# Kernel tuning notes

Measured on AMD Instinct MI355X. Metric: run time of the kernel, lower is better.

## Reference

```python
import jax, jax.numpy as jnp
import numpy as np

B, N, K, H = 4, 2048, 30, 128
NODE_IN, EDGE_IN, FF = 21, 16, 4 * H


def _normalize(t, axis=-1):
    d = t / jnp.linalg.norm(t, axis=axis, keepdims=True)
    return jnp.where(jnp.isnan(d), 0.0, d)


def gather_nodes(nodes, idx):
    # nodes: [B,N,C], idx: [B,N,K] -> [B,N,K,C]
    b, n, k = idx.shape
    flat = idx.reshape(b, n * k)
    out = jnp.take_along_axis(nodes, flat[:, :, None], axis=1)
    return out.reshape(b, n, k, nodes.shape[-1])


def cal_dihedral(Xf, eps=1e-7):
    dX = Xf[:, 1:, :] - Xf[:, :-1, :]
    U = _normalize(dX)
    u0, u1, u2 = U[:, :-2], U[:, 1:-1], U[:, 2:]
    n0 = _normalize(jnp.cross(u0, u1))
    n1 = _normalize(jnp.cross(u1, u2))
    cosD = jnp.clip((n0 * n1).sum(-1), -1 + eps, 1 - eps)
    v = _normalize(jnp.cross(n0, n1))
    return jnp.sign((-v * u1).sum(-1)) * jnp.arccos(cosD)


def dihedrals(X, eps=1e-7):
    b, n = X.shape[0], X.shape[1]
    Xf = X[:, :, :3, :].reshape(b, 3 * n, 3)
    D = cal_dihedral(Xf)
    D = jnp.pad(D, ((0, 0), (1, 2))).reshape(b, n, 3)
    dihed = jnp.concatenate([jnp.cos(D), jnp.sin(D)], -1)
    dX = Xf[:, 1:] - Xf[:, :-1]
    U = _normalize(dX)
    cosA = jnp.clip((U[:, :-2] * U[:, 1:-1]).sum(-1), -1 + eps, 1 - eps)
    A = jnp.pad(jnp.arccos(cosA), ((0, 0), (1, 2))).reshape(b, n, 3)
    ang = jnp.concatenate([jnp.cos(A), jnp.sin(A)], -1)
    return jnp.concatenate([dihed, ang], -1)  # [B,N,12]


def quaternions(R):
    diag = jnp.diagonal(R, axis1=-2, axis2=-1)
    Rxx, Ryy, Rzz = diag[..., 0], diag[..., 1], diag[..., 2]
    mags = 0.5 * jnp.sqrt(jnp.abs(1 + jnp.stack([Rxx - Ryy - Rzz, -Rxx + Ryy - Rzz, -Rxx - Ryy + Rzz], -1)))
    signs = jnp.sign(jnp.stack([R[..., 2, 1] - R[..., 1, 2], R[..., 0, 2] - R[..., 2, 0], R[..., 1, 0] - R[..., 0, 1]], -1))
    xyz = signs * mags
    w = jnp.sqrt(jax.nn.relu(1 + diag.sum(-1, keepdims=True))) / 2.0
    return _normalize(jnp.concatenate([xyz, w], -1))


def orientations(X, E_idx):
    V = X  # [B,N,4,3]
    b, n = X.shape[0], X.shape[1]
    k = E_idx.shape[2]
    Xf = X[:, :, :3, :].reshape(b, 3 * n, 3)
    dX = Xf[:, 1:] - Xf[:, :-1]
    U = _normalize(dX)
    u0, u1 = U[:, :-2], U[:, 1:-1]
    n0 = _normalize(jnp.cross(u0, u1))[:, ::3]
    b1 = _normalize(u0 - u1)[:, ::3]
    Xa = Xf[:, ::3]  # [B,N,3]
    Q = jnp.stack([b1, n0, jnp.cross(b1, n0)], 2)  # [B,N-1,3,3]
    Q = Q.reshape(b, Q.shape[1], 9)
    Q = jnp.pad(Q, ((0, 0), (0, 1), (0, 0)))  # [B,N,9]
    Qn = gather_nodes(Q, E_idx).reshape(b, n, k, 3, 3)
    Xn = gather_nodes(V[:, :, 1, :], E_idx)
    Nn = gather_nodes(V[:, :, 0, :], E_idx)
    Cn = gather_nodes(V[:, :, 2, :], E_idx)
    On = gather_nodes(V[:, :, 3, :], E_idx)
    Q3 = Q.reshape(b, n, 3, 3)
    dXn = jnp.stack([Xn, Nn, Cn, On], 3) - Xa[:, :, None, None, :]  # [B,N,K,4,3]
    dU = jnp.einsum('bnij,bnkaj->bnkai', Q3, dXn)
    E_direct = _normalize(dU).reshape(b, n, k, 12)
    R = jnp.einsum('bnji,bnkjl->bnkil', Q3, Qn)  # Q^T @ Q_neighbors
    q = quaternions(R)  # [B,N,K,4]
    dX_inner = V[:, :, jnp.array([0, 2, 3]), :] - Xa[:, :, None, :]
    dU_inner = _normalize(jnp.einsum('bnij,bnaj->bnai', Q3, dX_inner))
    V_direct = dU_inner.reshape(b, n, 9)
    return V_direct, E_direct, q


def layernorm(x, g, bta, eps=1e-5):
    m = x.mean(-1, keepdims=True)
    v = ((x - m) ** 2).mean(-1, keepdims=True)
    return (x - m) / jnp.sqrt(v + eps) * g + bta


def gelu(x):
    return jax.nn.gelu(x, approximate=False)


def forward(X, E_idx, Wv_w, Wv_b, We_w, We_b, W1_w, W1_b, W2_w, W2_b, W3_w, W3_b,
            Wi_w, Wi_b, Wo_w, Wo_b, ln1_g, ln1_b, ln2_g, ln2_b):
    k = E_idx.shape[2]
    Dfeat = dihedrals(X)                     # [B,N,12]
    Vd, Ed, q = orientations(X, E_idx)       # [B,N,9],[B,N,K,12],[B,N,K,4]
    hV = jnp.concatenate([Dfeat, Vd], -1) @ Wv_w + Wv_b     # [B,N,H]
    hE = jnp.concatenate([Ed, q], -1) @ We_w + We_b         # [B,N,K,H]
    hV_nbr = gather_nodes(hV, E_idx)                        # [B,N,K,H]
    hV_exp = jnp.broadcast_to(hV[:, :, None, :], hV_nbr.shape)
    hEV = jnp.concatenate([hV_exp, hE, hV_nbr], -1)         # [B,N,K,3H]
    msg = gelu(hEV @ W1_w + W1_b)
    msg = gelu(msg @ W2_w + W2_b)
    msg = msg @ W3_w + W3_b
    dh = msg.sum(-2) / k
    hV = layernorm(hV + dh, ln1_g, ln1_b)
    ff = gelu(hV @ Wi_w + Wi_b) @ Wo_w + Wo_b
    hV = layernorm(hV + ff, ln2_g, ln2_b)
    return hV


def _lin(key, fan_in, fan_out):
    s = 1.0 / np.sqrt(fan_in)
    kw, kb = jax.random.split(key)
    return (jax.random.uniform(kw, (fan_in, fan_out), minval=-s, maxval=s),
            jax.random.uniform(kb, (fan_out,), minval=-s, maxval=s))


def setup_inputs() -> dict:
    key = jax.random.key(0)
    ks = jax.random.split(key, 10)
    X = jax.random.normal(ks[0], (B, N, 4, 3), dtype=jnp.float32) * 3.0
    E_idx = jax.random.randint(ks[1], (B, N, K), 0, N)
    Wv_w, Wv_b = _lin(ks[2], NODE_IN, H)
    We_w, We_b = _lin(ks[3], EDGE_IN, H)
    W1_w, W1_b = _lin(ks[4], 3 * H, H)
    W2_w, W2_b = _lin(ks[5], H, H)
    W3_w, W3_b = _lin(ks[6], H, H)
    Wi_w, Wi_b = _lin(ks[7], H, FF)
    Wo_w, Wo_b = _lin(ks[8], FF, H)
    return {
        'X': X, 'E_idx': E_idx,
        'Wv_w': Wv_w, 'Wv_b': Wv_b, 'We_w': We_w, 'We_b': We_b,
        'W1_w': W1_w, 'W1_b': W1_b, 'W2_w': W2_w, 'W2_b': W2_b,
        'W3_w': W3_w, 'W3_b': W3_b, 'Wi_w': Wi_w, 'Wi_b': Wi_b,
        'Wo_w': Wo_w, 'Wo_b': Wo_b,
        'ln1_g': jnp.ones((H,), jnp.float32), 'ln1_b': jnp.zeros((H,), jnp.float32),
        'ln2_g': jnp.ones((H,), jnp.float32), 'ln2_b': jnp.zeros((H,), jnp.float32),
    }


def reference(X, E_idx, Wv_w, Wv_b, We_w, We_b, W1_w, W1_b, W2_w, W2_b, W3_w, W3_b,
              Wi_w, Wi_b, Wo_w, Wo_b, ln1_g, ln1_b, ln2_g, ln2_b):
    return forward(X, E_idx, Wv_w, Wv_b, We_w, We_b, W1_w, W1_b, W2_w, W2_b,
                   W3_w, W3_b, Wi_w, Wi_b, Wo_w, Wo_b, ln1_g, ln1_b, ln2_g, ln2_b)
```

## Files before the change

### kernel.cpp

```cpp
#include <hip/hip_runtime.h>
#include <math.h>

#define BB 4
#define NN 2048
#define KNB 30
#define HH 128
#define FFD 512

typedef __attribute__((ext_vector_type(4))) float  f32x4;
typedef __attribute__((ext_vector_type(8))) short  s16x8;
typedef __attribute__((ext_vector_type(4))) short  s16x4;

struct F3 { float x,y,z; };
__device__ __forceinline__ F3 f3(float a,float b,float c){ F3 r; r.x=a; r.y=b; r.z=c; return r; }
__device__ __forceinline__ F3 sub3(F3 a, F3 b){ return f3(a.x-b.x, a.y-b.y, a.z-b.z); }
__device__ __forceinline__ float dot3(F3 a, F3 b){ return a.x*b.x + a.y*b.y + a.z*b.z; }
__device__ __forceinline__ F3 cross3(F3 a, F3 b){
  return f3(a.y*b.z-a.z*b.y, a.z*b.x-a.x*b.z, a.x*b.y-a.y*b.x);
}
__device__ __forceinline__ F3 nrm3(F3 a){
  float n2 = dot3(a,a);
  if (n2 <= 0.f) return f3(0.f,0.f,0.f);
  float inv = 1.0f/sqrtf(n2);
  return f3(a.x*inv, a.y*inv, a.z*inv);
}
__device__ __forceinline__ float sgnf(float x){ return (x>0.f)?1.f:((x<0.f)?-1.f:0.f); }
__device__ __forceinline__ float clip1(float x){
  const float e = 1e-7f;
  return fminf(fmaxf(x, -1.f+e), 1.f-e);
}
__device__ __forceinline__ float fgelu(float x){
  float x2 = x*x;
  float t = __builtin_fmaf(-0.1029641763f, x2, -2.302344055f);
  float d = 1.f + __builtin_amdgcn_exp2f(t*x);
  return x * __builtin_amdgcn_rcpf(d);
}
__device__ __forceinline__ short f2bf(float x){
  union { float f; unsigned u; } v; v.f = x;
  unsigned r = v.u + 0x7fffu + ((v.u >> 16) & 1u);
  return (short)(r >> 16);
}

__global__ void k_init(const float* __restrict__ X, float* __restrict__ Qws,
                       float* __restrict__ featws,
                       const float* __restrict__ We, const float* __restrict__ Web,
                       const float* __restrict__ W1, const float* __restrict__ W2,
                       const float* __restrict__ Wi, const float* __restrict__ Wo,
                       short* __restrict__ wfoldT, float* __restrict__ bfold,
                       short* __restrict__ w2t, short* __restrict__ w1aT,
                       short* __restrict__ w1cT, short* __restrict__ wiT,
                       short* __restrict__ woT){
  if (blockIdx.x < 32){
    int t = blockIdx.x*256 + threadIdx.x;
    int b = t / NN, n = t % NN;
    const float* Xb = X + (size_t)b*NN*12;
    #define LD3(r,a) f3(Xb[((r)*4+(a))*3+0], Xb[((r)*4+(a))*3+1], Xb[((r)*4+(a))*3+2])
    F3 x0=LD3(n,0), x1=LD3(n,1), x2=LD3(n,2), x3=LD3(n,3);
    F3 U[5];
    U[1]=nrm3(sub3(x1,x0));
    U[2]=nrm3(sub3(x2,x1));
    if (n>0){ F3 p = LD3(n-1,2); U[0]=nrm3(sub3(x0,p)); } else U[0]=f3(0.f,0.f,0.f);
    if (n<NN-1){ F3 y0=LD3(n+1,0), y1=LD3(n+1,1); U[3]=nrm3(sub3(y0,x2)); U[4]=nrm3(sub3(y1,y0)); }
    else { U[3]=f3(0.f,0.f,0.f); U[4]=f3(0.f,0.f,0.f); }

    float feat[21];
    #pragma unroll
    for (int tt=0; tt<3; tt++){
      bool valid = (n>0 || tt>0) && (n<NN-1 || tt==0);
      if (valid){
        F3 a=U[tt], bv=U[tt+1], c=U[tt+2];
        F3 n0=nrm3(cross3(a,bv)), n1=nrm3(cross3(bv,c));
        float cd = clip1(dot3(n0,n1));
        F3 v = nrm3(cross3(n0,n1));
        float s = sgnf(-dot3(v,bv));
        feat[tt]   = (s==0.f) ? 1.f : cd;
        feat[3+tt] = s*sqrtf(fmaxf(1.f-cd*cd, 0.f));
        float ca = clip1(dot3(a,bv));
        feat[6+tt] = ca;
        feat[9+tt] = sqrtf(fmaxf(1.f-ca*ca, 0.f));
      } else {
        feat[tt]=1.f; feat[3+tt]=0.f; feat[6+tt]=1.f; feat[9+tt]=0.f;
      }
    }
    float Q[9];
    if (n<NN-1){
      F3 b1=nrm3(sub3(U[1],U[2]));
      F3 n0=nrm3(cross3(U[1],U[2]));
      F3 r2=cross3(b1,n0);
      Q[0]=b1.x;Q[1]=b1.y;Q[2]=b1.z;Q[3]=n0.x;Q[4]=n0.y;Q[5]=n0.z;Q[6]=r2.x;Q[7]=r2.y;Q[8]=r2.z;
    } else {
      #pragma unroll
      for (int i=0;i<9;i++) Q[i]=0.f;
    }
    float* qp = Qws + (size_t)t*9;
    #pragma unroll
    for (int i=0;i<9;i++) qp[i]=Q[i];

    feat[12]=0.f; feat[13]=0.f; feat[14]=0.f;
    F3 d1=sub3(x2,x0), d2=sub3(x3,x0);
    F3 r1 = nrm3(f3(Q[0]*d1.x+Q[1]*d1.y+Q[2]*d1.z,
                    Q[3]*d1.x+Q[4]*d1.y+Q[5]*d1.z,
                    Q[6]*d1.x+Q[7]*d1.y+Q[8]*d1.z));
    F3 r2v= nrm3(f3(Q[0]*d2.x+Q[1]*d2.y+Q[2]*d2.z,
                    Q[3]*d2.x+Q[4]*d2.y+Q[5]*d2.z,
                    Q[6]*d2.x+Q[7]*d2.y+Q[8]*d2.z));
    feat[15]=r1.x; feat[16]=r1.y; feat[17]=r1.z;
    feat[18]=r2v.x; feat[19]=r2v.y; feat[20]=r2v.z;
    float* fp = featws + (size_t)t*21;
    #pragma unroll
    for (int i=0;i<21;i++) fp[i]=feat[i];
    #undef LD3
    return;
  }
  int t = (blockIdx.x-32)*256 + threadIdx.x;
  if (t < 2048){
    int c = t >> 4, j = t & 15;
    float a = 0.f;
    for (int k=0;k<HH;k++) a += We[j*HH+k]*W1[(HH+k)*HH + c];
    wfoldT[t] = f2bf(a);
  } else if (t < 2176){
    int c = t - 2048;
    float a = 0.f;
    for (int k=0;k<HH;k++) a += Web[k]*W1[(HH+k)*HH + c];
    bfold[c] = a;
  } else if (t < 18560){
    int i = t - 2176;  int n = i >> 7, k = i & 127;
    w2t[n*HH + k] = f2bf(W2[k*HH + n]);
  } else if (t < 34944){
    int i = t - 18560; int n = i >> 7, k = i & 127;
    w1aT[n*HH + k] = f2bf(W1[k*HH + n]);
  } else if (t < 51328){
    int i = t - 34944; int n = i >> 7, k = i & 127;
    w1cT[n*HH + k] = f2bf(W1[(256+k)*HH + n]);
  } else if (t < 116864){
    int i = t - 51328; int n = i >> 7, k = i & 127;
    wiT[n*HH + k] = f2bf(Wi[k*FFD + n]);
  } else if (t < 182400){
    int i = t - 116864; int k = i >> 7, n = i & 127;
    woT[n*FFD + k] = f2bf(Wo[k*HH + n]);
  }
}

#define PNB 32
__global__ void k_pre(const float* __restrict__ featws, const float* __restrict__ Wv,
                      const float* __restrict__ Wvb, const short* __restrict__ w1aT,
                      const short* __restrict__ w1cT, const float* __restrict__ W1b,
                      const float* __restrict__ bfold, float* __restrict__ hVws,
                      float* __restrict__ Sws, float* __restrict__ Gws){
  __shared__ __align__(16) short hvL[PNB][136];
  int tid = threadIdx.x;
  int base = blockIdx.x*PNB;
  {
    int c = tid & 127, half = tid >> 7;
    float wv[21];
    #pragma unroll
    for (int j=0;j<21;j++) wv[j] = Wv[j*HH + c];
    float wb = Wvb[c];
    #pragma unroll 2
    for (int it=0; it<16; ++it){
      int g = it*2 + half;
      const float* f = featws + (size_t)(base+g)*21;
      float a = wb;
      #pragma unroll
      for (int j=0;j<21;j++) a += f[j]*wv[j];
      hVws[(size_t)(base+g)*HH + c] = a;
      hvL[g][c] = f2bf(a);
    }
  }
  __syncthreads();
  {
    int l = tid & 63, w = tid >> 6;
    int lr = l & 15, lg = l >> 4;
    int m = w & 1;
    int nbase = (w >> 1)*4;
    s16x8 afr[4];
    #pragma unroll
    for (int ks=0; ks<4; ks++)
      afr[ks] = *reinterpret_cast<const s16x8*>(&hvL[m*16 + lr][ks*32 + lg*8]);
    f32x4 Cs[4], Cg[4];
    #pragma unroll
    for (int q=0;q<4;q++){ Cs[q]=(f32x4){0,0,0,0}; Cg[q]=(f32x4){0,0,0,0}; }
    #pragma unroll
    for (int q=0;q<4;q++){
      int ncol = (nbase+q)*16 + lr;
      #pragma unroll
      for (int ks=0; ks<4; ks++){
        s16x8 ba = *reinterpret_cast<const s16x8*>(&w1aT[ncol*HH + ks*32 + lg*8]);
        s16x8 bc = *reinterpret_cast<const s16x8*>(&w1cT[ncol*HH + ks*32 + lg*8]);
        Cs[q] = __builtin_amdgcn_mfma_f32_16x16x32_bf16(afr[ks], ba, Cs[q], 0,0,0);
        Cg[q] = __builtin_amdgcn_mfma_f32_16x16x32_bf16(afr[ks], bc, Cg[q], 0,0,0);
      }
    }
    #pragma unroll
    for (int q=0;q<4;q++){
      int ncol = (nbase+q)*16 + lr;
      float bc = W1b[ncol] + bfold[ncol];
      #pragma unroll
      for (int i=0;i<4;i++){
        int row = m*16 + lg*4 + i;
        size_t o = (size_t)(base+row)*HH + ncol;
        Sws[o] = Cs[q][i] + bc;
        Gws[o] = Cg[q][i];
      }
    }
  }
}

#define NPB 4
#define A2STR 136
#define EFSTR 20
__launch_bounds__(256, 4)
__global__ void k_msg(const float* __restrict__ X, const int* __restrict__ Eidx,
                      const float* __restrict__ Qws, const float* __restrict__ Sws,
                      const float* __restrict__ Gws, const float* __restrict__ hVws,
                      const short* __restrict__ wfoldT, const short* __restrict__ w2t,
                      const float* __restrict__ W2b, const float* __restrict__ W3,
                      const float* __restrict__ W3b, float* __restrict__ xpre){
  __shared__ __align__(16) short efL[128*EFSTR];
  __shared__ int idxL[128];
  __shared__ __align__(16) short A2s[128*A2STR];
  float* csL = (float*)efL;

  const int tid = threadIdx.x;
  const int gbase = blockIdx.x*NPB;
  const int b = gbase >> 11;
  const int bofs = b*NN;

  if (tid < NPB*KNB){
    int nn = tid / KNB;
    int kk = tid - nn*KNB;
    int gnode = gbase + nn;
    int n = gnode - bofs;
    int j = Eidx[(size_t)gnode*KNB + kk];
    int r = nn*32 + kk;
    idxL[r] = j;
    const float* Qs = Qws + (size_t)gnode*9;
    float q[9];
    #pragma unroll
    for (int i=0;i<9;i++) q[i]=Qs[i];
    const float* Xb = X + (size_t)b*NN*12;
    F3 Xa = f3(Xb[n*12+0], Xb[n*12+1], Xb[n*12+2]);
    const float* Xn = Xb + (size_t)j*12;
    F3 A[4];
    A[0] = f3(Xn[3],  Xn[4],  Xn[5]);
    A[1] = f3(Xn[0],  Xn[1],  Xn[2]);
    A[2] = f3(Xn[6],  Xn[7],  Xn[8]);
    A[3] = f3(Xn[9],  Xn[10], Xn[11]);
    #pragma unroll
    for (int a=0;a<4;a++){
      F3 d = sub3(A[a], Xa);
      F3 w = f3(q[0]*d.x+q[1]*d.y+q[2]*d.z,
                q[3]*d.x+q[4]*d.y+q[5]*d.z,
                q[6]*d.x+q[7]*d.y+q[8]*d.z);
      F3 wn = nrm3(w);
      efL[r*EFSTR + a*3 + 0] = f2bf(wn.x);
      efL[r*EFSTR + a*3 + 1] = f2bf(wn.y);
      efL[r*EFSTR + a*3 + 2] = f2bf(wn.z);
    }
    const float* Qn = Qws + (size_t)(bofs + j)*9;
    float p[9];
    #pragma unroll
    for (int i=0;i<9;i++) p[i]=Qn[i];
    float R00=q[0]*p[0]+q[3]*p[3]+q[6]*p[6];
    float R01=q[0]*p[1]+q[3]*p[4]+q[6]*p[7];
    float R02=q[0]*p[2]+q[3]*p[5]+q[6]*p[8];
    float R10=q[1]*p[0]+q[4]*p[3]+q[7]*p[6];
    float R11=q[1]*p[1]+q[4]*p[4]+q[7]*p[7];
    float R12=q[1]*p[2]+q[4]*p[5]+q[7]*p[8];
    float R20=q[2]*p[0]+q[5]*p[3]+q[8]*p[6];
    float R21=q[2]*p[1]+q[5]*p[4]+q[8]*p[7];
    float R22=q[2]*p[2]+q[5]*p[5]+q[8]*p[8];
    float mx = 0.5f*sqrtf(fabsf(1.f+R00-R11-R22));
    float my = 0.5f*sqrtf(fabsf(1.f-R00+R11-R22));
    float mz = 0.5f*sqrtf(fabsf(1.f-R00-R11+R22));
    float qx = sgnf(R21-R12)*mx;
    float qy = sgnf(R02-R20)*my;
    float qz = sgnf(R10-R01)*mz;
    float qw = 0.5f*sqrtf(fmaxf(1.f+R00+R11+R22, 0.f));
    float n2 = qx*qx+qy*qy+qz*qz+qw*qw;
    float inv = (n2>0.f) ? 1.f/sqrtf(n2) : 0.f;
    efL[r*EFSTR+12]=f2bf(qx*inv); efL[r*EFSTR+13]=f2bf(qy*inv);
    efL[r*EFSTR+14]=f2bf(qz*inv); efL[r*EFSTR+15]=f2bf(qw*inv);
  } else if (tid < 128){
    int e = tid - 120;
    int nn = e >> 1, slot = 30 + (e & 1);
    int r = nn*32 + slot;
    idxL[r] = 0;
    #pragma unroll
    for (int j2=0;j2<16;j2++) efL[r*EFSTR + j2] = 0;
  }
  __syncthreads();

  const int w  = tid >> 6;
  const int l  = tid & 63;
  const int lr = l & 15;
  const int lg = l >> 4;

  {
    s16x8 wf[8];
    #pragma unroll
    for (int ct=0; ct<8; ct++){
      if (lg < 2)
        wf[ct] = *reinterpret_cast<const s16x8*>(&wfoldT[(ct*16+lr)*16 + lg*8]);
      else
        wf[ct] = (s16x8){0,0,0,0,0,0,0,0};
    }
    s16x8 ef[2];
    #pragma unroll
    for (int rt=0; rt<2; rt++){
      if (lg < 2){
        const short* p = &efL[(w*32 + rt*16 + lr)*EFSTR + lg*8];
        s16x4 lo = *reinterpret_cast<const s16x4*>(p);
        s16x4 hi = *reinterpret_cast<const s16x4*>(p+4);
        s16x8 v;
        #pragma unroll
        for (int j2=0;j2<4;j2++){ v[j2]=lo[j2]; v[4+j2]=hi[j2]; }
        ef[rt] = v;
      } else {
        ef[rt] = (s16x8){0,0,0,0,0,0,0,0};
      }
    }
    const int e0 = w*32 + lr;
    const int e1 = e0 + 16;
    const bool ok1 = (lr < KNB - 16);
    const float* g0 = Gws + (size_t)(bofs + idxL[e0])*HH;
    const float* g1 = Gws + (size_t)(bofs + idxL[e1])*HH;
    const float* Srow = Sws + (size_t)(gbase+w)*HH;
    #pragma unroll
    for (int ct=0; ct<8; ct++){
      const int cbase = ct*16 + lg*4;
      f32x4 S4 = *reinterpret_cast<const f32x4*>(Srow + cbase);
      f32x4 G0 = *reinterpret_cast<const f32x4*>(g0 + cbase);
      f32x4 G1 = *reinterpret_cast<const f32x4*>(g1 + cbase);
      f32x4 C0 = __builtin_amdgcn_mfma_f32_16x16x32_bf16(wf[ct], ef[0], (f32x4){0,0,0,0}, 0,0,0);
      f32x4 C1 = __builtin_amdgcn_mfma_f32_16x16x32_bf16(wf[ct], ef[1], (f32x4){0,0,0,0}, 0,0,0);
      s16x4 o0, o1;
      #pragma unroll
      for (int i=0;i<4;i++){
        o0[i] = f2bf(fgelu(C0[i] + S4[i] + G0[i]));
        float v1 = fgelu(C1[i] + S4[i] + G1[i]);
        o1[i] = ok1 ? f2bf(v1) : (short)0;
      }
      *reinterpret_cast<s16x4*>(&A2s[e0*A2STR + cbase]) = o0;
      *reinterpret_cast<s16x4*>(&A2s[e1*A2STR + cbase]) = o1;
    }
  }
  __syncthreads();

  {
    f32x4 Cacc[2][8];
    #pragma unroll
    for (int mt=0; mt<2; mt++)
      #pragma unroll
      for (int nt=0; nt<8; nt++)
        Cacc[mt][nt] = (f32x4){0.f,0.f,0.f,0.f};
    #pragma unroll
    for (int ks=0; ks<4; ks++){
      const int koff = ks*32 + lg*8;
      s16x8 a0 = *reinterpret_cast<const s16x8*>(&A2s[(w*32      + lr)*A2STR + koff]);
      s16x8 a1 = *reinterpret_cast<const s16x8*>(&A2s[(w*32 + 16 + lr)*A2STR + koff]);
      #pragma unroll
      for (int nt=0; nt<8; nt++){
        s16x8 bv = *reinterpret_cast<const s16x8*>(&w2t[(lr + nt*16)*HH + koff]);
        Cacc[0][nt] = __builtin_amdgcn_mfma_f32_16x16x32_bf16(a0, bv, Cacc[0][nt], 0,0,0);
        Cacc[1][nt] = __builtin_amdgcn_mfma_f32_16x16x32_bf16(a1, bv, Cacc[1][nt], 0,0,0);
      }
    }
    #pragma unroll
    for (int nt=0; nt<8; nt++){
      float b2v = W2b[lr + nt*16];
      float part = 0.f;
      #pragma unroll
      for (int mt=0; mt<2; mt++){
        #pragma unroll
        for (int i=0; i<4; i++){
          int row32 = mt*16 + lg*4 + i;
          float v = fgelu(Cacc[mt][nt][i] + b2v);
          if (row32 < KNB) part += v;
        }
      }
      part += __shfl_xor(part, 16, 64);
      part += __shfl_xor(part, 32, 64);
      if (l < 16) csL[w*HH + nt*16 + lr] = part;
    }
  }
  __syncthreads();

  {
    const int h = tid & 127;
    const int half = tid >> 7;
    #pragma unroll
    for (int q2=0; q2<2; q2++){
      int nn = half*2 + q2;
      const float* cs = csL + nn*HH;
      float acc = 0.f;
      for (int j=0;j<HH;j+=4){
        acc += cs[j]  *W3[(j  )*HH+h] + cs[j+1]*W3[(j+1)*HH+h]
             + cs[j+2]*W3[(j+2)*HH+h] + cs[j+3]*W3[(j+3)*HH+h];
      }
      size_t o = (size_t)(gbase + nn)*HH + h;
      xpre[o] = hVws[o] + acc*(1.f/30.f) + W3b[h];
    }
  }
}

#define FNB 16
__global__ void k_ffn(const float* __restrict__ xpre, const short* __restrict__ wiT,
                      const short* __restrict__ woT, const float* __restrict__ Wib,
                      const float* __restrict__ Wob, const float* __restrict__ l1g,
                      const float* __restrict__ l1b, const float* __restrict__ l2g,
                      const float* __restrict__ l2b, float* __restrict__ out){
  __shared__ __align__(16) short hv1[FNB][136];
  __shared__ __align__(16) float yL[FNB][HH];
  __shared__ __align__(16) short ffh[FNB][520];
  __shared__ float partS[FNB][4], partQ[FNB][4];
  const int tid = threadIdx.x;
  const int l = tid & 63, w = tid >> 6;
  const int base = blockIdx.x*FNB;

  #pragma unroll
  for (int ri=0; ri<4; ri++){
    int r = w*4 + ri;
    const float* xp = xpre + (size_t)(base+r)*HH;
    float x0 = xp[l], x1 = xp[l+64];
    float s = x0 + x1;
    #pragma unroll
    for (int o=32;o>0;o>>=1) s += __shfl_xor(s, o, 64);
    float mean = s*(1.f/HH);
    float d0 = x0-mean, d1 = x1-mean;
    float q = d0*d0 + d1*d1;
    #pragma unroll
    for (int o=32;o>0;o>>=1) q += __shfl_xor(q, o, 64);
    float inv = 1.f/sqrtf(q*(1.f/HH) + 1e-5f);
    float y0 = d0*inv*l1g[l]    + l1b[l];
    float y1 = d1*inv*l1g[l+64] + l1b[l+64];
    yL[r][l] = y0; yL[r][l+64] = y1;
    hv1[r][l] = f2bf(y0); hv1[r][l+64] = f2bf(y1);
  }
  __syncthreads();

  const int lr = l & 15, lg = l >> 4;
  {
    s16x8 afr[4];
    #pragma unroll
    for (int ks=0; ks<4; ks++)
      afr[ks] = *reinterpret_cast<const s16x8*>(&hv1[lr][ks*32 + lg*8]);
    #pragma unroll
    for (int q=0; q<8; q++){
      int ncol = (w*8+q)*16 + lr;
      f32x4 C = (f32x4){0,0,0,0};
      #pragma unroll
      for (int ks=0; ks<4; ks++){
        s16x8 bv = *reinterpret_cast<const s16x8*>(&wiT[ncol*HH + ks*32 + lg*8]);
        C = __builtin_amdgcn_mfma_f32_16x16x32_bf16(afr[ks], bv, C, 0,0,0);
      }
      float bi = Wib[ncol];
      #pragma unroll
      for (int i=0;i<4;i++){
        int row = lg*4 + i;
        ffh[row][ncol] = f2bf(fgelu(C[i] + bi));
      }
    }
  }
  __syncthreads();

  f32x4 C2[2];
  C2[0]=(f32x4){0,0,0,0}; C2[1]=(f32x4){0,0,0,0};
  for (int ks=0; ks<16; ++ks){
    s16x8 a = *reinterpret_cast<const s16x8*>(&ffh[lr][ks*32 + lg*8]);
    #pragma unroll
    for (int t2=0; t2<2; t2++){
      int ncol = (2*w+t2)*16 + lr;
      s16x8 bv = *reinterpret_cast<const s16x8*>(&woT[ncol*FFD + ks*32 + lg*8]);
      C2[t2] = __builtin_amdgcn_mfma_f32_16x16x32_bf16(a, bv, C2[t2], 0,0,0);
    }
  }
  float vv[2][4];
  float ps[4] = {0,0,0,0}, pq[4] = {0,0,0,0};
  #pragma unroll
  for (int t2=0; t2<2; t2++){
    int col = (2*w+t2)*16 + lr;
    float bo = Wob[col];
    #pragma unroll
    for (int i=0;i<4;i++){
      int row = lg*4 + i;
      float v = yL[row][col] + C2[t2][i] + bo;
      vv[t2][i] = v;
      ps[i] += v; pq[i] += v*v;
    }
  }
  #pragma unroll
  for (int i=0;i<4;i++){
    #pragma unroll
    for (int o=1;o<16;o<<=1){
      ps[i] += __shfl_xor(ps[i], o, 64);
      pq[i] += __shfl_xor(pq[i], o, 64);
    }
    if (lr == 0){ partS[lg*4+i][w] = ps[i]; partQ[lg*4+i][w] = pq[i]; }
  }
  __syncthreads();
  float mean[4], inv[4];
  #pragma unroll
  for (int i=0;i<4;i++){
    int row = lg*4 + i;
    float S = partS[row][0]+partS[row][1]+partS[row][2]+partS[row][3];
    float Q = partQ[row][0]+partQ[row][1]+partQ[row][2]+partQ[row][3];
    float m = S*(1.f/HH);
    float var = Q*(1.f/HH) - m*m;
    mean[i] = m;
    inv[i] = 1.f/sqrtf(var + 1e-5f);
  }
  #pragma unroll
  for (int t2=0; t2<2; t2++){
    int col = (2*w+t2)*16 + lr;
    float g2 = l2g[col], b2 = l2b[col];
    #pragma unroll
    for (int i=0;i<4;i++){
      int row = lg*4 + i;
      out[(size_t)(base+row)*HH + col] = (vv[t2][i]-mean[i])*inv[i]*g2 + b2;
    }
  }
}

extern "C" void kernel_launch(void* const* d_in, const int* in_sizes, int n_in,
                              void* d_out, int out_size, void* d_ws, size_t ws_size,
                              hipStream_t stream) {
  (void)in_sizes; (void)n_in; (void)out_size; (void)ws_size;
  const float* X   = (const float*)d_in[0];
  const int*   Ei  = (const int*)  d_in[1];
  const float* Wv  = (const float*)d_in[2];
  const float* Wvb = (const float*)d_in[3];
  const float* We  = (const float*)d_in[4];
  const float* Web = (const float*)d_in[5];
  const float* W1  = (const float*)d_in[6];
  const float* W1b = (const float*)d_in[7];
  const float* W2  = (const float*)d_in[8];
  const float* W2b = (const float*)d_in[9];
  const float* W3  = (const float*)d_in[10];
  const float* W3b = (const float*)d_in[11];
  const float* Wi  = (const float*)d_in[12];
  const float* Wib = (const float*)d_in[13];
  const float* Wo  = (const float*)d_in[14];
  const float* Wob = (const float*)d_in[15];
  const float* l1g = (const float*)d_in[16];
  const float* l1b = (const float*)d_in[17];
  const float* l2g = (const float*)d_in[18];
  const float* l2b = (const float*)d_in[19];
  float* out = (float*)d_out;

  float* wsf    = (float*)d_ws;
  float* featws = wsf + 0;
  float* Qws    = wsf + 172032;
  float* hVws   = wsf + 245760;
  float* Gws    = wsf + 1294336;
  float* Sws    = wsf + 2342912;
  float* xprews = Sws;
  short* wfoldT = (short*)(wsf + 3391488);
  float* bfold  = wsf + 3392512;
  short* w2t    = (short*)(wsf + 3392640);
  short* w1aT   = (short*)(wsf + 3400832);
  short* w1cT   = (short*)(wsf + 3409024);
  short* wiT    = (short*)(wsf + 3417216);
  short* woT    = (short*)(wsf + 3449984);

  k_init<<<dim3(745), dim3(256), 0, stream>>>(X, Qws, featws, We, Web, W1, W2, Wi, Wo,
                                              wfoldT, bfold, w2t, w1aT, w1cT, wiT, woT);
  k_pre <<<dim3(BB*NN/PNB), dim3(256), 0, stream>>>(featws, Wv, Wvb, w1aT, w1cT,
                                                    W1b, bfold, hVws, Sws, Gws);
  k_msg <<<dim3(BB*NN/NPB), dim3(256), 0, stream>>>(X, Ei, Qws, Sws, Gws, hVws,
                                                    wfoldT, w2t, W2b, W3, W3b, xprews);
  k_ffn <<<dim3(BB*NN/FNB), dim3(256), 0, stream>>>(xprews, wiT, woT, Wib, Wob,
                                                    l1g, l1b, l2g, l2b, out);
}
```

Baseline: 204.0 us.

## Move W3 projection from message kernel into FFN kernel as bf16 MFMA

The per-node W3 matmul and residual add leave k_msg, which now writes only the neighbor-summed message vector to a workspace. k_ffn loads these sums, runs the W3 projection on MFMA with a pre-transposed bf16 W3, adds hV and the bias, and computes LayerNorm from cross-wave partial sums. This removes a scalar fp32 matvec with an extra barrier from k_msg and batches it over 16 nodes on the matrix cores. In exchange the message sums are rounded to bf16 and the variance is computed as E[x²]-m², which costs some precision.

```diff
diff --git a/kernel.cpp b/kernel.cpp
--- a/kernel.cpp
+++ b/kernel.cpp
@@ -46,10 +46,11 @@
                        const float* __restrict__ We, const float* __restrict__ Web,
                        const float* __restrict__ W1, const float* __restrict__ W2,
                        const float* __restrict__ Wi, const float* __restrict__ Wo,
+                       const float* __restrict__ W3,
                        short* __restrict__ wfoldT, float* __restrict__ bfold,
                        short* __restrict__ w2t, short* __restrict__ w1aT,
                        short* __restrict__ w1cT, short* __restrict__ wiT,
-                       short* __restrict__ woT){
+                       short* __restrict__ woT, short* __restrict__ w3T){
   if (blockIdx.x < 32){
     int t = blockIdx.x*256 + threadIdx.x;
     int b = t / NN, n = t % NN;
@@ -138,6 +139,9 @@
   } else if (t < 182400){
     int i = t - 116864; int k = i >> 7, n = i & 127;
     woT[n*FFD + k] = f2bf(Wo[k*HH + n]);
+  } else if (t < 198784){
+    int i = t - 182400; int n = i >> 7, k = i & 127;
+    w3T[n*HH + k] = f2bf(W3[k*HH + n]);
   }
 }
 
@@ -212,14 +216,12 @@
 __launch_bounds__(256, 4)
 __global__ void k_msg(const float* __restrict__ X, const int* __restrict__ Eidx,
                       const float* __restrict__ Qws, const float* __restrict__ Sws,
-                      const float* __restrict__ Gws, const float* __restrict__ hVws,
+                      const float* __restrict__ Gws,
                       const short* __restrict__ wfoldT, const short* __restrict__ w2t,
-                      const float* __restrict__ W2b, const float* __restrict__ W3,
-                      const float* __restrict__ W3b, float* __restrict__ xpre){
+                      const float* __restrict__ W2b, float* __restrict__ csws){
   __shared__ __align__(16) short efL[128*EFSTR];
   __shared__ int idxL[128];
   __shared__ __align__(16) short A2s[128*A2STR];
-  float* csL = (float*)efL;
 
   const int tid = threadIdx.x;
   const int gbase = blockIdx.x*NPB;
@@ -366,6 +368,7 @@
         Cacc[1][nt] = __builtin_amdgcn_mfma_f32_16x16x32_bf16(a1, bv, Cacc[1][nt], 0,0,0);
       }
     }
+    float* csrow = csws + (size_t)(gbase+w)*HH;
     #pragma unroll
     for (int nt=0; nt<8; nt++){
       float b2v = W2b[lr + nt*16];
@@ -381,35 +384,19 @@
       }
       part += __shfl_xor(part, 16, 64);
       part += __shfl_xor(part, 32, 64);
-      if (l < 16) csL[w*HH + nt*16 + lr] = part;
-    }
-  }
-  __syncthreads();
-
-  {
-    const int h = tid & 127;
-    const int half = tid >> 7;
-    #pragma unroll
-    for (int q2=0; q2<2; q2++){
-      int nn = half*2 + q2;
-      const float* cs = csL + nn*HH;
-      float acc = 0.f;
-      for (int j=0;j<HH;j+=4){
-        acc += cs[j]  *W3[(j  )*HH+h] + cs[j+1]*W3[(j+1)*HH+h]
-             + cs[j+2]*W3[(j+2)*HH+h] + cs[j+3]*W3[(j+3)*HH+h];
-      }
-      size_t o = (size_t)(gbase + nn)*HH + h;
-      xpre[o] = hVws[o] + acc*(1.f/30.f) + W3b[h];
+      if (l < 16) csrow[nt*16 + lr] = part;
     }
   }
 }
 
 #define FNB 16
-__global__ void k_ffn(const float* __restrict__ xpre, const short* __restrict__ wiT,
-                      const short* __restrict__ woT, const float* __restrict__ Wib,
-                      const float* __restrict__ Wob, const float* __restrict__ l1g,
-                      const float* __restrict__ l1b, const float* __restrict__ l2g,
-                      const float* __restrict__ l2b, float* __restrict__ out){
+__global__ void k_ffn(const float* __restrict__ csws, const float* __restrict__ hVws,
+                      const short* __restrict__ w3T, const float* __restrict__ W3b,
+                      const short* __restrict__ wiT, const short* __restrict__ woT,
+                      const float* __restrict__ Wib, const float* __restrict__ Wob,
+                      const float* __restrict__ l1g, const float* __restrict__ l1b,
+                      const float* __restrict__ l2g, const float* __restrict__ l2b,
+                      float* __restrict__ out){
   __shared__ __align__(16) short hv1[FNB][136];
   __shared__ __align__(16) float yL[FNB][HH];
   __shared__ __align__(16) short ffh[FNB][520];
@@ -417,29 +404,80 @@
   const int tid = threadIdx.x;
   const int l = tid & 63, w = tid >> 6;
   const int base = blockIdx.x*FNB;
-
-  #pragma unroll
-  for (int ri=0; ri<4; ri++){
-    int r = w*4 + ri;
-    const float* xp = xpre + (size_t)(base+r)*HH;
-    float x0 = xp[l], x1 = xp[l+64];
-    float s = x0 + x1;
-    #pragma unroll
-    for (int o=32;o>0;o>>=1) s += __shfl_xor(s, o, 64);
-    float mean = s*(1.f/HH);
-    float d0 = x0-mean, d1 = x1-mean;
-    float q = d0*d0 + d1*d1;
-    #pragma unroll
-    for (int o=32;o>0;o>>=1) q += __shfl_xor(q, o, 64);
-    float inv = 1.f/sqrtf(q*(1.f/HH) + 1e-5f);
-    float y0 = d0*inv*l1g[l]    + l1b[l];
-    float y1 = d1*inv*l1g[l+64] + l1b[l+64];
-    yL[r][l] = y0; yL[r][l+64] = y1;
-    hv1[r][l] = f2bf(y0); hv1[r][l+64] = f2bf(y1);
+  const int lr = l & 15, lg = l >> 4;
+
+  {
+    int i0 = tid*8;
+    int row = i0 >> 7, col = i0 & 127;
+    const float* p = csws + (size_t)(base+row)*HH + col;
+    f32x4 a = *reinterpret_cast<const f32x4*>(p);
+    f32x4 bq = *reinterpret_cast<const f32x4*>(p+4);
+    s16x8 v;
+    #pragma unroll
+    for (int j=0;j<4;j++){ v[j]=f2bf(a[j]); v[4+j]=f2bf(bq[j]); }
+    *reinterpret_cast<s16x8*>(&hv1[row][col]) = v;
   }
   __syncthreads();
 
-  const int lr = l & 15, lg = l >> 4;
+  {
+    s16x8 acs[4];
+    #pragma unroll
+    for (int ks=0; ks<4; ks++)
+      acs[ks] = *reinterpret_cast<const s16x8*>(&hv1[lr][ks*32 + lg*8]);
+    f32x4 Cd[2];
+    Cd[0]=(f32x4){0,0,0,0}; Cd[1]=(f32x4){0,0,0,0};
+    #pragma unroll
+    for (int t2=0; t2<2; t2++){
+      int ncol = (2*w+t2)*16 + lr;
+      #pragma unroll
+      for (int ks=0; ks<4; ks++){
+        s16x8 bv = *reinterpret_cast<const s16x8*>(&w3T[ncol*HH + ks*32 + lg*8]);
+        Cd[t2] = __builtin_amdgcn_mfma_f32_16x16x32_bf16(acs[ks], bv, Cd[t2], 0,0,0);
+      }
+    }
+    float vv[2][4];
+    float ps[4] = {0,0,0,0}, pq[4] = {0,0,0,0};
+    #pragma unroll
+    for (int t2=0; t2<2; t2++){
+      int col = (2*w+t2)*16 + lr;
+      float b3 = W3b[col];
+      #pragma unroll
+      for (int i=0;i<4;i++){
+        int row = lg*4 + i;
+        float v = hVws[(size_t)(base+row)*HH + col] + Cd[t2][i]*(1.f/30.f) + b3;
+        vv[t2][i] = v;
+        ps[i] += v; pq[i] += v*v;
+      }
+    }
+    #pragma unroll
+    for (int i=0;i<4;i++){
+      #pragma unroll
+      for (int o=1;o<16;o<<=1){
+        ps[i] += __shfl_xor(ps[i], o, 64);
+        pq[i] += __shfl_xor(pq[i], o, 64);
+      }
+      if (lr == 0){ partS[lg*4+i][w] = ps[i]; partQ[lg*4+i][w] = pq[i]; }
+    }
+    __syncthreads();
+    #pragma unroll
+    for (int t2=0; t2<2; t2++){
+      int col = (2*w+t2)*16 + lr;
+      float g1 = l1g[col], b1 = l1b[col];
+      #pragma unroll
+      for (int i=0;i<4;i++){
+        int row = lg*4 + i;
+        float S = partS[row][0]+partS[row][1]+partS[row][2]+partS[row][3];
+        float Q = partQ[row][0]+partQ[row][1]+partQ[row][2]+partQ[row][3];
+        float m = S*(1.f/HH);
+        float inv = 1.f/sqrtf(Q*(1.f/HH) - m*m + 1e-5f);
+        float y = (vv[t2][i]-m)*inv*g1 + b1;
+        yL[row][col] = y;
+        hv1[row][col] = f2bf(y);
+      }
+    }
+  }
+  __syncthreads();
+
   {
     s16x8 afr[4];
     #pragma unroll
@@ -554,21 +592,22 @@
   float* hVws   = wsf + 245760;
   float* Gws    = wsf + 1294336;
   float* Sws    = wsf + 2342912;
-  float* xprews = Sws;
-  short* wfoldT = (short*)(wsf + 3391488);
-  float* bfold  = wsf + 3392512;
-  short* w2t    = (short*)(wsf + 3392640);
-  short* w1aT   = (short*)(wsf + 3400832);
-  short* w1cT   = (short*)(wsf + 3409024);
-  short* wiT    = (short*)(wsf + 3417216);
-  short* woT    = (short*)(wsf + 3449984);
-
-  k_init<<<dim3(745), dim3(256), 0, stream>>>(X, Qws, featws, We, Web, W1, W2, Wi, Wo,
-                                              wfoldT, bfold, w2t, w1aT, w1cT, wiT, woT);
+  float* csws   = wsf + 3391488;
+  short* wfoldT = (short*)(wsf + 4440064);
+  float* bfold  = wsf + 4441088;
+  short* w2t    = (short*)(wsf + 4441216);
+  short* w1aT   = (short*)(wsf + 4449408);
+  short* w1cT   = (short*)(wsf + 4457600);
+  short* wiT    = (short*)(wsf + 4465792);
+  short* woT    = (short*)(wsf + 4498560);
+  short* w3T    = (short*)(wsf + 4531328);
+
+  k_init<<<dim3(809), dim3(256), 0, stream>>>(X, Qws, featws, We, Web, W1, W2, Wi, Wo, W3,
+                                              wfoldT, bfold, w2t, w1aT, w1cT, wiT, woT, w3T);
   k_pre <<<dim3(BB*NN/PNB), dim3(256), 0, stream>>>(featws, Wv, Wvb, w1aT, w1cT,
                                                     W1b, bfold, hVws, Sws, Gws);
-  k_msg <<<dim3(BB*NN/NPB), dim3(256), 0, stream>>>(X, Ei, Qws, Sws, Gws, hVws,
-                                                    wfoldT, w2t, W2b, W3, W3b, xprews);
-  k_ffn <<<dim3(BB*NN/FNB), dim3(256), 0, stream>>>(xprews, wiT, woT, Wib, Wob,
-                                                    l1g, l1b, l2g, l2b, out);
-}
+  k_msg <<<dim3(BB*NN/NPB), dim3(256), 0, stream>>>(X, Ei, Qws, Sws, Gws,
+                                                    wfoldT, w2t, W2b, csws);
+  k_ffn <<<dim3(BB*NN/FNB), dim3(256), 0, stream>>>(csws, hVws, w3T, W3b, wiT, woT,
+                                                    Wib, Wob, l1g, l1b, l2g, l2b, out);
+}
```

New measurement: 192.6 us. 5.6% less time.
